# Kernel tuning notes

Hardware: AMD Instinct MI355X
Metric: run time of the kernel (lower is better)

Reference implementation:

```python
import jax, jax.numpy as jnp
import numpy as np

PUSH_MARGIN = 0.25


def setup_inputs() -> dict:
    key = jax.random.key(0)
    k1, k2 = jax.random.split(key)
    B, H, W, D, K = 8, 512, 512, 32, 64
    embeddings = jax.random.normal(k1, (B, H, W, D), dtype=jnp.float32)
    labels = jax.random.randint(k2, (B, H, W), 0, K, dtype=jnp.int32)
    return {"embeddings": embeddings, "labels": labels, "n_instances": K}


def _metric_loss(embeddings, labels, n_instances):
    # embeddings: (B, H, W, D) float; labels: (B, H, W) int; n_instances: static int K
    B = embeddings.shape[0]
    D = embeddings.shape[-1]
    K = n_instances
    emb = embeddings.reshape(B, -1, D)          # (B, N, D)
    lab = labels.reshape(B, -1).astype(jnp.int32)  # (B, N)

    # One-pass segment reduce over all batches: offset labels per batch element.
    seg = (lab + jnp.arange(B, dtype=jnp.int32)[:, None] * K).reshape(-1)  # (B*N,)
    sums = jax.ops.segment_sum(emb.reshape(-1, D), seg, num_segments=B * K)
    counts = jax.ops.segment_sum(jnp.ones(seg.shape, dtype=emb.dtype), seg,
                                 num_segments=B * K)
    sums = sums.reshape(B, K, D)
    counts = counts.reshape(B, K)
    present = counts > 0.5                       # non-empty instances (B, K)
    centroids = sums / jnp.maximum(counts, 1.0)[..., None]  # (B, K, D); zeros if empty

    # Pairwise Manhattan distances between centroids: (B, K, K)
    dist = jnp.sum(jnp.abs(centroids[:, :, None, :] - centroids[:, None, :, :]), axis=-1)
    hinge = jax.nn.relu(PUSH_MARGIN - dist)      # push: relu(margin - d)
    sq = hinge * hinge                           # squared error metric

    # strictly upper triangular + only pairs of non-empty instances
    triu = jnp.triu(jnp.ones((K, K), dtype=bool), k=1)
    pair_mask = triu[None] & present[:, :, None] & present[:, None, :]
    per_image_sum = jnp.sum(jnp.where(pair_mask, sq, 0.0), axis=(1, 2))  # (B,)

    n = jnp.sum(present.astype(emb.dtype), axis=1)              # (B,) non-empty count
    n_comparisons = n * (n - 1.0) / 2.0
    push_loss = per_image_sum / n_comparisons
    return jnp.mean(push_loss)


def reference(embeddings, labels, n_instances):
    return _metric_loss(embeddings, labels, n_instances)
```

## Files before the change

kernel.cpp:

```cpp
#include <hip/hip_runtime.h>

#define B_    8
#define N_    (512 * 512)
#define D_    32
#define K_    64
#define TPB   256
#define NWAVE (TPB / 64)
#define KROW  36
#define TABW  (K_ * KROW)
#define REC   (K_ * D_ + K_)
#define RECQ  (REC / 4)

#define PROC(L0,L1,L2,L3,L4,L5,L6,L7, V, PBASE)                               \
  {                                                                           \
    int lb = egl < 4 ? (egl < 2 ? (egl == 0 ? L0 : L1)                        \
                                : (egl == 2 ? L2 : L3))                       \
                     : (egl < 6 ? (egl == 4 ? L4 : L5)                        \
                                : (egl == 6 ? L6 : L7));                      \
    const int m0 = (lb == L0), m1 = (lb == L1), m2 = (lb == L2),              \
              m3 = (lb == L3), m4 = (lb == L4), m5 = (lb == L5),              \
              m6 = (lb == L6), m7 = (lb == L7);                               \
    const int order = (g0 & m0) + (g1 & m1) + (g2 & m2) + (g3 & m3) +         \
                      (g4 & m4) + (g5 & m5) + (g6 & m6);                      \
    const int nsame = m0 + m1 + m2 + m3 + m4 + m5 + m6 + m7;                  \
    const float4 vc = V;                                                      \
    const int pb = (PBASE);                                                   \
    if (pb < N_) {                                        \
      const int* lp = lab + bbase + pb + wb;      \
      L0 = lp[0]; L1 = lp[1]; L2 = lp[2]; L3 = lp[3];                         \
      L4 = lp[4]; L5 = lp[5]; L6 = lp[6]; L7 = lp[7];                         \
      V = embv[(bbase + pb + eg) * 8 + d4];                                   \
    }                                                                         \
    const int a = lb * KROW + d4 * 4;                                         \
    if (order == 0) {                                                         \
      float4 cur = *reinterpret_cast<const float4*>(tab + a);                 \
      cur.x += vc.x; cur.y += vc.y; cur.z += vc.z; cur.w += vc.w;             \
      *reinterpret_cast<float4*>(tab + a) = cur;                              \
      if (d4 == 0) cnt[lb] += (float)nsame;                                   \
    } else {                  \
      atomicAdd(&tab[a + 0], vc.x);                                           \
      atomicAdd(&tab[a + 1], vc.y);                                           \
      atomicAdd(&tab[a + 2], vc.z);                                           \
      atomicAdd(&tab[a + 3], vc.w);                                           \
    }                                                                         \
  }

__global__ __launch_bounds__(TPB) void seg_partial_kernel(
    const float* __restrict__ emb, const int* __restrict__ lab,
    float* __restrict__ partials, int blk_per_b)
{
    __shared__ __align__(16) float s_tab[NWAVE * TABW];
    __shared__ float s_cnt[NWAVE * K_];

    for (int i = threadIdx.x; i < NWAVE * TABW; i += TPB) s_tab[i] = 0.f;
    for (int i = threadIdx.x; i < NWAVE * K_;  i += TPB) s_cnt[i] = 0.f;
    __syncthreads();

    const int tid  = threadIdx.x;
    const int wave = tid >> 6;
    const int lane = tid & 63;
    const int egl  = lane >> 3;
    const int d4   = lane & 7;
    const int eg   = wave * 8 + egl;

    const int g0 = (0 < egl), g1 = (1 < egl), g2 = (2 < egl), g3 = (3 < egl),
              g4 = (4 < egl), g5 = (5 < egl), g6 = (6 < egl);

    float* __restrict__ tab = s_tab + wave * TABW;
    float* __restrict__ cnt = s_cnt + wave * K_;

    const int blk = blockIdx.x;
    const int b   = blk / blk_per_b;
    const int bib = blk - b * blk_per_b;
    const long long bbase = (long long)b * N_;
    const float4* __restrict__ embv = reinterpret_cast<const float4*>(emb);
    const int STEP = blk_per_b * 32;
    const int wb = __builtin_amdgcn_readfirstlane(wave * 8);

    int ib = bib * 32;

    int a0, a1, a2, a3, a4, a5, a6, a7;
    float4 va;
    {
        const int* lp = lab + bbase + ib + wb;
        a0 = lp[0]; a1 = lp[1]; a2 = lp[2]; a3 = lp[3];
        a4 = lp[4]; a5 = lp[5]; a6 = lp[6]; a7 = lp[7];
        va = embv[(bbase + ib + eg) * 8 + d4];
    }
    int b0 = 0, b1 = 0, b2 = 0, b3 = 0, b4 = 0, b5 = 0, b6 = 0, b7 = 0;
    float4 vb = make_float4(0.f, 0.f, 0.f, 0.f);
    if (ib + STEP < N_) {
        const int* lp = lab + bbase + ib + STEP + wb;
        b0 = lp[0]; b1 = lp[1]; b2 = lp[2]; b3 = lp[3];
        b4 = lp[4]; b5 = lp[5]; b6 = lp[6]; b7 = lp[7];
        vb = embv[(bbase + ib + STEP + eg) * 8 + d4];
    }

    for (;;) {
        PROC(a0, a1, a2, a3, a4, a5, a6, a7, va, ib + 2 * STEP);
        ib += STEP;
        if (ib >= N_) break;
        PROC(b0, b1, b2, b3, b4, b5, b6, b7, vb, ib + 2 * STEP);
        ib += STEP;
        if (ib >= N_) break;
    }
    __syncthreads();

    float* out = partials + (size_t)blk * REC;
    for (int i = tid; i < K_ * D_; i += TPB) {
        int k = i >> 5, d = i & 31;
        float s = 0.f;
#pragma unroll
        for (int w = 0; w < NWAVE; ++w) s += s_tab[w * TABW + k * KROW + d];
        out[i] = s;
    }
    if (tid < K_) {
        float c = 0.f;
#pragma unroll
        for (int w = 0; w < NWAVE; ++w) c += s_cnt[w * K_ + tid];
        out[K_ * D_ + tid] = c;
    }
}

__global__ __launch_bounds__(TPB) void seg_reduce_a(
    const float* __restrict__ partials, float* __restrict__ part2,
    int rpc, int nch)
{
    const int blk = blockIdx.x;
    const int b   = blk / nch;
    const int ch  = blk - b * nch;
    const int tid = threadIdx.x;

    const float4* __restrict__ p4 = reinterpret_cast<const float4*>(partials)
        + (size_t)((b * nch + ch) * rpc) * RECQ;
    float4* __restrict__ o4 = reinterpret_cast<float4*>(part2)
        + (size_t)blk * RECQ;

    float4 acc0 = make_float4(0.f, 0.f, 0.f, 0.f);
    float4 acc1 = acc0, acc2 = acc0;
#pragma unroll 4
    for (int r = 0; r < rpc; ++r) {
        const float4* rp = p4 + (size_t)r * RECQ;
        float4 v0 = rp[tid];
        float4 v1 = rp[tid + 256];
        acc0.x += v0.x; acc0.y += v0.y; acc0.z += v0.z; acc0.w += v0.w;
        acc1.x += v1.x; acc1.y += v1.y; acc1.z += v1.z; acc1.w += v1.w;
        if (tid < 16) {
            float4 v2 = rp[tid + 512];
            acc2.x += v2.x; acc2.y += v2.y; acc2.z += v2.z; acc2.w += v2.w;
        }
    }
    o4[tid]       = acc0;
    o4[tid + 256] = acc1;
    if (tid < 16) o4[tid + 512] = acc2;
}

__global__ __launch_bounds__(TPB) void loss8_kernel(
    const float* __restrict__ part2, float* __restrict__ batch_loss,
    int nch)
{
    __shared__ __align__(16) float4 s_cent4[8 * K_];
    __shared__ float s_cntsh[K_];
    __shared__ float s_pres[K_];
    __shared__ float s_wred[NWAVE];

    const int b   = blockIdx.x;
    const int tid = threadIdx.x;
    const float4* __restrict__ p4 = reinterpret_cast<const float4*>(part2)
        + (size_t)(b * nch) * RECQ;

    float4 acc0 = make_float4(0.f, 0.f, 0.f, 0.f);
    float4 acc1 = acc0, acc2 = acc0;
#pragma unroll 8
    for (int c = 0; c < nch; ++c) {
        const float4* rp = p4 + (size_t)c * RECQ;
        float4 v0 = rp[tid];
        float4 v1 = rp[tid + 256];
        acc0.x += v0.x; acc0.y += v0.y; acc0.z += v0.z; acc0.w += v0.w;
        acc1.x += v1.x; acc1.y += v1.y; acc1.z += v1.z; acc1.w += v1.w;
        if (tid < 16) {
            float4 v2 = rp[tid + 512];
            acc2.x += v2.x; acc2.y += v2.y; acc2.z += v2.z; acc2.w += v2.w;
        }
    }

    s_cent4[(tid & 7) * K_ + (tid >> 3)] = acc0;
    {
        const int q1 = tid + 256;
        s_cent4[(q1 & 7) * K_ + (q1 >> 3)] = acc1;
    }
    if (tid < 16) reinterpret_cast<float4*>(s_cntsh)[tid] = acc2;
    __syncthreads();

    if (tid < K_) s_pres[tid] = (s_cntsh[tid] > 0.5f) ? 1.f : 0.f;
    for (int i = tid; i < 8 * K_; i += TPB) {
        float inv = 1.0f / fmaxf(s_cntsh[i & 63], 1.0f);
        float4 c = s_cent4[i];
        c.x *= inv; c.y *= inv; c.z *= inv; c.w *= inv;
        s_cent4[i] = c;
    }
    __syncthreads();

    const int wave = tid >> 6, lane = tid & 63;

    float4 cb[8];
#pragma unroll
    for (int j = 0; j < 8; ++j) cb[j] = s_cent4[j * K_ + lane];
    const float pres2 = s_pres[lane];

    float acc = 0.f;
#pragma unroll 4
    for (int t = 0; t < 16; ++t) {
        const int k1 = wave * 16 + t;
        float dist = 0.f;
#pragma unroll
        for (int j = 0; j < 8; ++j) {
            float4 a = s_cent4[j * K_ + k1];
            dist += fabsf(a.x - cb[j].x) + fabsf(a.y - cb[j].y)
                  + fabsf(a.z - cb[j].z) + fabsf(a.w - cb[j].w);
        }
        float h = fmaxf(0.25f - dist, 0.f);
        float valid = (k1 < lane) ? s_pres[k1] * pres2 : 0.f;
        acc += valid * h * h;
    }
#pragma unroll
    for (int m = 32; m > 0; m >>= 1) acc += __shfl_xor(acc, m);
    if (lane == 0) s_wred[wave] = acc;
    __syncthreads();
    if (tid == 0) {
        float s = s_wred[0] + s_wred[1] + s_wred[2] + s_wred[3];
        float n = 0.f;
        for (int k = 0; k < K_; ++k) n += s_pres[k];
        float ncomp = n * (n - 1.f) * 0.5f;
        batch_loss[b] = (ncomp > 0.f) ? (s / ncomp) : 0.f;
    }
}

__global__ void final_kernel(const float* __restrict__ batch_loss,
                             float* __restrict__ out)
{
    if (threadIdx.x == 0) {
        float t = 0.f;
#pragma unroll
        for (int b = 0; b < B_; ++b) t += batch_loss[b];
        out[0] = t * (1.0f / (float)B_);
    }
}

extern "C" void kernel_launch(void* const* d_in, const int* in_sizes, int n_in,
                              void* d_out, int out_size, void* d_ws, size_t ws_size,
                              hipStream_t stream)
{
    const float* emb = (const float*)d_in[0];
    const int*   lab = (const int*)d_in[1];
    float*       out = (float*)d_out;
    float*       ws  = (float*)d_ws;

    int blk_per_b = 128;
    while (blk_per_b > 8) {
        size_t need = ((size_t)(blk_per_b * B_) * REC
                       + (size_t)(B_ * 8) * REC
                       + B_) * sizeof(float);
        if (need <= ws_size) break;
        blk_per_b >>= 1;
    }
    const int nblk = blk_per_b * B_;
    const int nch  = (blk_per_b >= 8) ? 8 : blk_per_b;
    const int rpc  = blk_per_b / nch;

    float* partials   = ws;
    float* part2      = ws + (size_t)nblk * REC;
    float* batch_loss = part2 + (size_t)(B_ * nch) * REC;

    seg_partial_kernel<<<nblk, TPB, 0, stream>>>(emb, lab, partials, blk_per_b);

    seg_reduce_a<<<B_ * nch, TPB, 0, stream>>>(partials, part2, rpc, nch);

    loss8_kernel<<<B_, TPB, 0, stream>>>(part2, batch_loss, nch);

    final_kernel<<<1, 64, 0, stream>>>(batch_loss, out);
}
```

Measured before the change: 74.72 us.

## Share shared-memory histogram tables between wave pairs and double blocks per batch

Each pair of waves now covers 16 pixels with 4 lanes per pixel per wave (the two waves split the 32 dims), so a block keeps two private centroid tables instead of four. This halves LDS usage, and together with launch_bounds(256,8) it is meant to raise occupancy. Counting moves to a per-pixel atomicAdd from a single designated lane, replacing the per-run count accumulation. Blocks per batch double to 256, which adds more partial records for the reduce stage to read. In exchange, the 16-way duplicate detection costs more ALU work and more label registers per thread.

```diff
diff --git a/kernel.cpp b/kernel.cpp
--- a/kernel.cpp
+++ b/kernel.cpp
@@ -6,37 +6,45 @@
 #define K_    64
 #define TPB   256
 #define NWAVE (TPB / 64)
+#define NPAIR (TPB / 128)
 #define KROW  36
 #define TABW  (K_ * KROW)
 #define REC   (K_ * D_ + K_)
 #define RECQ  (REC / 4)
 
-#define PROC(L0,L1,L2,L3,L4,L5,L6,L7, V, PBASE)                               \
+#define PROC16(L0,L1,L2,L3,L4,L5,L6,L7,L8,L9,L10,L11,L12,L13,L14,L15, V, PBASE) \
   {                                                                           \
-    int lb = egl < 4 ? (egl < 2 ? (egl == 0 ? L0 : L1)                        \
-                                : (egl == 2 ? L2 : L3))                       \
-                     : (egl < 6 ? (egl == 4 ? L4 : L5)                        \
-                                : (egl == 6 ? L6 : L7));                      \
-    const int m0 = (lb == L0), m1 = (lb == L1), m2 = (lb == L2),              \
-              m3 = (lb == L3), m4 = (lb == L4), m5 = (lb == L5),              \
-              m6 = (lb == L6), m7 = (lb == L7);                               \
+    int lb = el < 8                                                           \
+      ? (el < 4 ? (el < 2 ? (el == 0 ? L0 : L1) : (el == 2 ? L2 : L3))        \
+                : (el < 6 ? (el == 4 ? L4 : L5) : (el == 6 ? L6 : L7)))       \
+      : (el < 12 ? (el < 10 ? (el == 8 ? L8 : L9) : (el == 10 ? L10 : L11))   \
+                 : (el < 14 ? (el == 12 ? L12 : L13)                          \
+                            : (el == 14 ? L14 : L15)));                       \
+    const int m0 = (lb == L0),  m1 = (lb == L1),  m2 = (lb == L2),            \
+              m3 = (lb == L3),  m4 = (lb == L4),  m5 = (lb == L5),            \
+              m6 = (lb == L6),  m7 = (lb == L7),  m8 = (lb == L8),            \
+              m9 = (lb == L9),  m10 = (lb == L10), m11 = (lb == L11),         \
+              m12 = (lb == L12), m13 = (lb == L13), m14 = (lb == L14);        \
     const int order = (g0 & m0) + (g1 & m1) + (g2 & m2) + (g3 & m3) +         \
-                      (g4 & m4) + (g5 & m5) + (g6 & m6);                      \
-    const int nsame = m0 + m1 + m2 + m3 + m4 + m5 + m6 + m7;                  \
+                      (g4 & m4) + (g5 & m5) + (g6 & m6) + (g7 & m7) +         \
+                      (g8 & m8) + (g9 & m9) + (g10 & m10) + (g11 & m11) +     \
+                      (g12 & m12) + (g13 & m13) + (g14 & m14);                \
     const float4 vc = V;                                                      \
     const int pb = (PBASE);                                                   \
     if (pb < N_) {                                        \
       const int* lp = lab + bbase + pb + wb;      \
-      L0 = lp[0]; L1 = lp[1]; L2 = lp[2]; L3 = lp[3];                         \
-      L4 = lp[4]; L5 = lp[5]; L6 = lp[6]; L7 = lp[7];                         \
+      L0 = lp[0];  L1 = lp[1];  L2 = lp[2];  L3 = lp[3];                      \
+      L4 = lp[4];  L5 = lp[5];  L6 = lp[6];  L7 = lp[7];                      \
+      L8 = lp[8];  L9 = lp[9];  L10 = lp[10]; L11 = lp[11];                   \
+      L12 = lp[12]; L13 = lp[13]; L14 = lp[14]; L15 = lp[15];                 \
       V = embv[(bbase + pb + eg) * 8 + d4];                                   \
     }                                                                         \
     const int a = lb * KROW + d4 * 4;                                         \
+    if (czen) atomicAdd(&cnt[lb], 1.0f);                                      \
     if (order == 0) {                                                         \
       float4 cur = *reinterpret_cast<const float4*>(tab + a);                 \
       cur.x += vc.x; cur.y += vc.y; cur.z += vc.z; cur.w += vc.w;             \
       *reinterpret_cast<float4*>(tab + a) = cur;                              \
-      if (d4 == 0) cnt[lb] += (float)nsame;                                   \
     } else {                  \
       atomicAdd(&tab[a + 0], vc.x);                                           \
       atomicAdd(&tab[a + 1], vc.y);                                           \
@@ -45,29 +53,46 @@
     }                                                                         \
   }
 
-__global__ __launch_bounds__(TPB) void seg_partial_kernel(
+#define LOADSET16(L0,L1,L2,L3,L4,L5,L6,L7,L8,L9,L10,L11,L12,L13,L14,L15, V, BASE) \
+  if ((BASE) < N_) {                                                          \
+    const int* lp = lab + bbase + (BASE) + wb;                                \
+    L0 = lp[0];  L1 = lp[1];  L2 = lp[2];  L3 = lp[3];                        \
+    L4 = lp[4];  L5 = lp[5];  L6 = lp[6];  L7 = lp[7];                        \
+    L8 = lp[8];  L9 = lp[9];  L10 = lp[10]; L11 = lp[11];                     \
+    L12 = lp[12]; L13 = lp[13]; L14 = lp[14]; L15 = lp[15];                   \
+    V = embv[(bbase + (BASE) + eg) * 8 + d4];                                 \
+  }
+
+__global__ __launch_bounds__(TPB, 8) void seg_partial_kernel(
     const float* __restrict__ emb, const int* __restrict__ lab,
     float* __restrict__ partials, int blk_per_b)
 {
-    __shared__ __align__(16) float s_tab[NWAVE * TABW];
-    __shared__ float s_cnt[NWAVE * K_];
-
-    for (int i = threadIdx.x; i < NWAVE * TABW; i += TPB) s_tab[i] = 0.f;
-    for (int i = threadIdx.x; i < NWAVE * K_;  i += TPB) s_cnt[i] = 0.f;
+    __shared__ __align__(16) float s_tab[NPAIR * TABW];
+    __shared__ float s_cnt[NPAIR * K_];
+
+    for (int i = threadIdx.x; i < NPAIR * TABW; i += TPB) s_tab[i] = 0.f;
+    for (int i = threadIdx.x; i < NPAIR * K_;  i += TPB) s_cnt[i] = 0.f;
     __syncthreads();
 
     const int tid  = threadIdx.x;
     const int wave = tid >> 6;
+    const int pair = wave >> 1;
+    const int hi   = wave & 1;
     const int lane = tid & 63;
-    const int egl  = lane >> 3;
-    const int d4   = lane & 7;
-    const int eg   = wave * 8 + egl;
-
-    const int g0 = (0 < egl), g1 = (1 < egl), g2 = (2 < egl), g3 = (3 < egl),
-              g4 = (4 < egl), g5 = (5 < egl), g6 = (6 < egl);
-
-    float* __restrict__ tab = s_tab + wave * TABW;
-    float* __restrict__ cnt = s_cnt + wave * K_;
+    const int el   = lane >> 2;
+    const int q    = lane & 3;
+    const int d4   = q + 4 * hi;
+    const int eg   = pair * 16 + el;
+    const int czen = (hi == 0) && (q == 0);
+
+    const int g0 = (0 < el),  g1 = (1 < el),  g2 = (2 < el),  g3 = (3 < el),
+              g4 = (4 < el),  g5 = (5 < el),  g6 = (6 < el),  g7 = (7 < el),
+              g8 = (8 < el),  g9 = (9 < el),  g10 = (10 < el),
+              g11 = (11 < el), g12 = (12 < el), g13 = (13 < el),
+              g14 = (14 < el);
+
+    float* __restrict__ tab = s_tab + pair * TABW;
+    float* __restrict__ cnt = s_cnt + pair * K_;
 
     const int blk = blockIdx.x;
     const int b   = blk / blk_per_b;
@@ -75,32 +100,26 @@
     const long long bbase = (long long)b * N_;
     const float4* __restrict__ embv = reinterpret_cast<const float4*>(emb);
     const int STEP = blk_per_b * 32;
-    const int wb = __builtin_amdgcn_readfirstlane(wave * 8);
+    const int wb = __builtin_amdgcn_readfirstlane(pair * 16);
 
     int ib = bib * 32;
 
-    int a0, a1, a2, a3, a4, a5, a6, a7;
-    float4 va;
-    {
-        const int* lp = lab + bbase + ib + wb;
-        a0 = lp[0]; a1 = lp[1]; a2 = lp[2]; a3 = lp[3];
-        a4 = lp[4]; a5 = lp[5]; a6 = lp[6]; a7 = lp[7];
-        va = embv[(bbase + ib + eg) * 8 + d4];
-    }
-    int b0 = 0, b1 = 0, b2 = 0, b3 = 0, b4 = 0, b5 = 0, b6 = 0, b7 = 0;
-    float4 vb = make_float4(0.f, 0.f, 0.f, 0.f);
-    if (ib + STEP < N_) {
-        const int* lp = lab + bbase + ib + STEP + wb;
-        b0 = lp[0]; b1 = lp[1]; b2 = lp[2]; b3 = lp[3];
-        b4 = lp[4]; b5 = lp[5]; b6 = lp[6]; b7 = lp[7];
-        vb = embv[(bbase + ib + STEP + eg) * 8 + d4];
-    }
+    int a0 = 0, a1 = 0, a2 = 0, a3 = 0, a4 = 0, a5 = 0, a6 = 0, a7 = 0,
+        a8 = 0, a9 = 0, a10 = 0, a11 = 0, a12 = 0, a13 = 0, a14 = 0, a15 = 0;
+    int b0 = 0, b1 = 0, b2 = 0, b3 = 0, b4 = 0, b5 = 0, b6 = 0, b7 = 0,
+        b8 = 0, b9 = 0, b10 = 0, b11 = 0, b12 = 0, b13 = 0, b14 = 0, b15 = 0;
+    float4 va = make_float4(0.f, 0.f, 0.f, 0.f), vb = va;
+    LOADSET16(a0,a1,a2,a3,a4,a5,a6,a7,a8,a9,a10,a11,a12,a13,a14,a15, va, ib);
+    LOADSET16(b0,b1,b2,b3,b4,b5,b6,b7,b8,b9,b10,b11,b12,b13,b14,b15, vb,
+              ib + STEP);
 
     for (;;) {
-        PROC(a0, a1, a2, a3, a4, a5, a6, a7, va, ib + 2 * STEP);
+        PROC16(a0,a1,a2,a3,a4,a5,a6,a7,a8,a9,a10,a11,a12,a13,a14,a15, va,
+               ib + 2 * STEP);
         ib += STEP;
         if (ib >= N_) break;
-        PROC(b0, b1, b2, b3, b4, b5, b6, b7, vb, ib + 2 * STEP);
+        PROC16(b0,b1,b2,b3,b4,b5,b6,b7,b8,b9,b10,b11,b12,b13,b14,b15, vb,
+               ib + 2 * STEP);
         ib += STEP;
         if (ib >= N_) break;
     }
@@ -111,13 +130,13 @@
         int k = i >> 5, d = i & 31;
         float s = 0.f;
 #pragma unroll
-        for (int w = 0; w < NWAVE; ++w) s += s_tab[w * TABW + k * KROW + d];
+        for (int w = 0; w < NPAIR; ++w) s += s_tab[w * TABW + k * KROW + d];
         out[i] = s;
     }
     if (tid < K_) {
         float c = 0.f;
 #pragma unroll
-        for (int w = 0; w < NWAVE; ++w) c += s_cnt[w * K_ + tid];
+        for (int w = 0; w < NPAIR; ++w) c += s_cnt[w * K_ + tid];
         out[K_ * D_ + tid] = c;
     }
 }
@@ -256,7 +275,7 @@
     float*       out = (float*)d_out;
     float*       ws  = (float*)d_ws;
 
-    int blk_per_b = 128;
+    int blk_per_b = 256;
     while (blk_per_b > 8) {
         size_t need = ((size_t)(blk_per_b * B_) * REC
                        + (size_t)(B_ * 8) * REC
```

Result: slower. 107.5 us (+43.9%).

## Fuse reduce and loss kernels into one kernel using last-block atomic counters

Applied to the files above, without the earlier changes.

Merges the partial segment-sum, the two-level reduction, the per-image loss and the final mean into one kernel. Global atomic counters with threadfences pick the last-arriving block of each group to do the next reduction stage. This removes three extra kernel launches and the gaps between them, but adds a memset launch plus serialized tail work inside the last blocks.

```diff
diff --git a/kernel.cpp b/kernel.cpp
--- a/kernel.cpp
+++ b/kernel.cpp
@@ -10,6 +10,7 @@
 #define TABW  (K_ * KROW)
 #define REC   (K_ * D_ + K_)
 #define RECQ  (REC / 4)
+#define NGRP  (B_ * 8)
 
 #define PROC(L0,L1,L2,L3,L4,L5,L6,L7, V, PBASE)                               \
   {                                                                           \
@@ -45,12 +46,15 @@
     }                                                                         \
   }
 
-__global__ __launch_bounds__(TPB) void seg_partial_kernel(
+__global__ __launch_bounds__(TPB) void mono_kernel(
     const float* __restrict__ emb, const int* __restrict__ lab,
-    float* __restrict__ partials, int blk_per_b)
+    float* __restrict__ partials, float* __restrict__ part2,
+    float* __restrict__ batch_loss, int* __restrict__ counters,
+    float* __restrict__ out, int blk_per_b)
 {
     __shared__ __align__(16) float s_tab[NWAVE * TABW];
     __shared__ float s_cnt[NWAVE * K_];
+    __shared__ int   s_role;
 
     for (int i = threadIdx.x; i < NWAVE * TABW; i += TPB) s_tab[i] = 0.f;
     for (int i = threadIdx.x; i < NWAVE * K_;  i += TPB) s_cnt[i] = 0.f;
@@ -106,143 +110,149 @@
     }
     __syncthreads();
 
-    float* out = partials + (size_t)blk * REC;
+    float* outp = partials + (size_t)blk * REC;
     for (int i = tid; i < K_ * D_; i += TPB) {
         int k = i >> 5, d = i & 31;
         float s = 0.f;
 #pragma unroll
         for (int w = 0; w < NWAVE; ++w) s += s_tab[w * TABW + k * KROW + d];
-        out[i] = s;
+        outp[i] = s;
     }
     if (tid < K_) {
         float c = 0.f;
 #pragma unroll
         for (int w = 0; w < NWAVE; ++w) c += s_cnt[w * K_ + tid];
-        out[K_ * D_ + tid] = c;
-    }
-}
-
-__global__ __launch_bounds__(TPB) void seg_reduce_a(
-    const float* __restrict__ partials, float* __restrict__ part2,
-    int rpc, int nch)
-{
-    const int blk = blockIdx.x;
-    const int b   = blk / nch;
-    const int ch  = blk - b * nch;
-    const int tid = threadIdx.x;
-
-    const float4* __restrict__ p4 = reinterpret_cast<const float4*>(partials)
-        + (size_t)((b * nch + ch) * rpc) * RECQ;
-    float4* __restrict__ o4 = reinterpret_cast<float4*>(part2)
-        + (size_t)blk * RECQ;
-
-    float4 acc0 = make_float4(0.f, 0.f, 0.f, 0.f);
-    float4 acc1 = acc0, acc2 = acc0;
+        outp[K_ * D_ + tid] = c;
+    }
+
+    const int gsize = blk_per_b >> 3;
+    const int g     = blk / gsize;
+
+    __syncthreads();
+    if (tid == 0) {
+        __threadfence();
+        s_role = (atomicAdd(&counters[g], 1) == gsize - 1);
+    }
+    __syncthreads();
+    if (!s_role) return;
+    __threadfence();
+
+    {
+        const float4* __restrict__ p4 = reinterpret_cast<const float4*>(partials)
+            + (size_t)(g * gsize) * RECQ;
+        float4* __restrict__ o4 = reinterpret_cast<float4*>(part2)
+            + (size_t)g * RECQ;
+        float4 acc0 = make_float4(0.f, 0.f, 0.f, 0.f);
+        float4 acc1 = acc0, acc2 = acc0;
 #pragma unroll 4
-    for (int r = 0; r < rpc; ++r) {
-        const float4* rp = p4 + (size_t)r * RECQ;
-        float4 v0 = rp[tid];
-        float4 v1 = rp[tid + 256];
-        acc0.x += v0.x; acc0.y += v0.y; acc0.z += v0.z; acc0.w += v0.w;
-        acc1.x += v1.x; acc1.y += v1.y; acc1.z += v1.z; acc1.w += v1.w;
-        if (tid < 16) {
-            float4 v2 = rp[tid + 512];
-            acc2.x += v2.x; acc2.y += v2.y; acc2.z += v2.z; acc2.w += v2.w;
-        }
-    }
-    o4[tid]       = acc0;
-    o4[tid + 256] = acc1;
-    if (tid < 16) o4[tid + 512] = acc2;
-}
-
-__global__ __launch_bounds__(TPB) void loss8_kernel(
-    const float* __restrict__ part2, float* __restrict__ batch_loss,
-    int nch)
-{
-    __shared__ __align__(16) float4 s_cent4[8 * K_];
-    __shared__ float s_cntsh[K_];
-    __shared__ float s_pres[K_];
-    __shared__ float s_wred[NWAVE];
-
-    const int b   = blockIdx.x;
-    const int tid = threadIdx.x;
-    const float4* __restrict__ p4 = reinterpret_cast<const float4*>(part2)
-        + (size_t)(b * nch) * RECQ;
-
-    float4 acc0 = make_float4(0.f, 0.f, 0.f, 0.f);
-    float4 acc1 = acc0, acc2 = acc0;
+        for (int r = 0; r < gsize; ++r) {
+            const float4* rp = p4 + (size_t)r * RECQ;
+            float4 v0 = rp[tid];
+            float4 v1 = rp[tid + 256];
+            acc0.x += v0.x; acc0.y += v0.y; acc0.z += v0.z; acc0.w += v0.w;
+            acc1.x += v1.x; acc1.y += v1.y; acc1.z += v1.z; acc1.w += v1.w;
+            if (tid < 16) {
+                float4 v2 = rp[tid + 512];
+                acc2.x += v2.x; acc2.y += v2.y; acc2.z += v2.z; acc2.w += v2.w;
+            }
+        }
+        o4[tid]       = acc0;
+        o4[tid + 256] = acc1;
+        if (tid < 16) o4[tid + 512] = acc2;
+    }
+    __syncthreads();
+    if (tid == 0) {
+        __threadfence();
+        s_role = (atomicAdd(&counters[NGRP + b], 1) == 7);
+    }
+    __syncthreads();
+    if (!s_role) return;
+    __threadfence();
+
+    {
+        float4* s_cent4 = reinterpret_cast<float4*>(s_tab);
+        float*  s_cntsh = s_tab + 2048;
+        float*  s_pres  = s_tab + 2112;
+        float*  s_wred  = s_tab + 2176;
+
+        const float4* __restrict__ p4 = reinterpret_cast<const float4*>(part2)
+            + (size_t)(b * 8) * RECQ;
+
+        float4 acc0 = make_float4(0.f, 0.f, 0.f, 0.f);
+        float4 acc1 = acc0, acc2 = acc0;
 #pragma unroll 8
-    for (int c = 0; c < nch; ++c) {
-        const float4* rp = p4 + (size_t)c * RECQ;
-        float4 v0 = rp[tid];
-        float4 v1 = rp[tid + 256];
-        acc0.x += v0.x; acc0.y += v0.y; acc0.z += v0.z; acc0.w += v0.w;
-        acc1.x += v1.x; acc1.y += v1.y; acc1.z += v1.z; acc1.w += v1.w;
-        if (tid < 16) {
-            float4 v2 = rp[tid + 512];
-            acc2.x += v2.x; acc2.y += v2.y; acc2.z += v2.z; acc2.w += v2.w;
-        }
-    }
-
-    s_cent4[(tid & 7) * K_ + (tid >> 3)] = acc0;
-    {
-        const int q1 = tid + 256;
-        s_cent4[(q1 & 7) * K_ + (q1 >> 3)] = acc1;
-    }
-    if (tid < 16) reinterpret_cast<float4*>(s_cntsh)[tid] = acc2;
-    __syncthreads();
-
-    if (tid < K_) s_pres[tid] = (s_cntsh[tid] > 0.5f) ? 1.f : 0.f;
-    for (int i = tid; i < 8 * K_; i += TPB) {
-        float inv = 1.0f / fmaxf(s_cntsh[i & 63], 1.0f);
-        float4 c = s_cent4[i];
-        c.x *= inv; c.y *= inv; c.z *= inv; c.w *= inv;
-        s_cent4[i] = c;
-    }
-    __syncthreads();
-
-    const int wave = tid >> 6, lane = tid & 63;
-
-    float4 cb[8];
-#pragma unroll
-    for (int j = 0; j < 8; ++j) cb[j] = s_cent4[j * K_ + lane];
-    const float pres2 = s_pres[lane];
-
-    float acc = 0.f;
+        for (int c = 0; c < 8; ++c) {
+            const float4* rp = p4 + (size_t)c * RECQ;
+            float4 v0 = rp[tid];
+            float4 v1 = rp[tid + 256];
+            acc0.x += v0.x; acc0.y += v0.y; acc0.z += v0.z; acc0.w += v0.w;
+            acc1.x += v1.x; acc1.y += v1.y; acc1.z += v1.z; acc1.w += v1.w;
+            if (tid < 16) {
+                float4 v2 = rp[tid + 512];
+                acc2.x += v2.x; acc2.y += v2.y; acc2.z += v2.z; acc2.w += v2.w;
+            }
+        }
+        __syncthreads();
+
+        s_cent4[(tid & 7) * K_ + (tid >> 3)] = acc0;
+        {
+            const int q1 = tid + 256;
+            s_cent4[(q1 & 7) * K_ + (q1 >> 3)] = acc1;
+        }
+        if (tid < 16) reinterpret_cast<float4*>(s_cntsh)[tid] = acc2;
+        __syncthreads();
+
+        if (tid < K_) s_pres[tid] = (s_cntsh[tid] > 0.5f) ? 1.f : 0.f;
+        for (int i = tid; i < 8 * K_; i += TPB) {
+            float inv = 1.0f / fmaxf(s_cntsh[i & 63], 1.0f);
+            float4 c = s_cent4[i];
+            c.x *= inv; c.y *= inv; c.z *= inv; c.w *= inv;
+            s_cent4[i] = c;
+        }
+        __syncthreads();
+
+        float4 cb[8];
+#pragma unroll
+        for (int j = 0; j < 8; ++j) cb[j] = s_cent4[j * K_ + lane];
+        const float pres2 = s_pres[lane];
+
+        float acc = 0.f;
 #pragma unroll 4
-    for (int t = 0; t < 16; ++t) {
-        const int k1 = wave * 16 + t;
-        float dist = 0.f;
-#pragma unroll
-        for (int j = 0; j < 8; ++j) {
-            float4 a = s_cent4[j * K_ + k1];
-            dist += fabsf(a.x - cb[j].x) + fabsf(a.y - cb[j].y)
-                  + fabsf(a.z - cb[j].z) + fabsf(a.w - cb[j].w);
-        }
-        float h = fmaxf(0.25f - dist, 0.f);
-        float valid = (k1 < lane) ? s_pres[k1] * pres2 : 0.f;
-        acc += valid * h * h;
-    }
-#pragma unroll
-    for (int m = 32; m > 0; m >>= 1) acc += __shfl_xor(acc, m);
-    if (lane == 0) s_wred[wave] = acc;
-    __syncthreads();
+        for (int t = 0; t < 16; ++t) {
+            const int k1 = wave * 16 + t;
+            float dist = 0.f;
+#pragma unroll
+            for (int j = 0; j < 8; ++j) {
+                float4 a = s_cent4[j * K_ + k1];
+                dist += fabsf(a.x - cb[j].x) + fabsf(a.y - cb[j].y)
+                      + fabsf(a.z - cb[j].z) + fabsf(a.w - cb[j].w);
+            }
+            float h = fmaxf(0.25f - dist, 0.f);
+            float valid = (k1 < lane) ? s_pres[k1] * pres2 : 0.f;
+            acc += valid * h * h;
+        }
+#pragma unroll
+        for (int m = 32; m > 0; m >>= 1) acc += __shfl_xor(acc, m);
+        if (lane == 0) s_wred[wave] = acc;
+        __syncthreads();
+        if (tid == 0) {
+            float s = s_wred[0] + s_wred[1] + s_wred[2] + s_wred[3];
+            float n = 0.f;
+            for (int k = 0; k < K_; ++k) n += s_pres[k];
+            float ncomp = n * (n - 1.f) * 0.5f;
+            batch_loss[b] = (ncomp > 0.f) ? (s / ncomp) : 0.f;
+            __threadfence();
+            s_role = (atomicAdd(&counters[NGRP + B_], 1) == B_ - 1);
+        }
+    }
+    __syncthreads();
+    if (!s_role) return;
+
     if (tid == 0) {
-        float s = s_wred[0] + s_wred[1] + s_wred[2] + s_wred[3];
-        float n = 0.f;
-        for (int k = 0; k < K_; ++k) n += s_pres[k];
-        float ncomp = n * (n - 1.f) * 0.5f;
-        batch_loss[b] = (ncomp > 0.f) ? (s / ncomp) : 0.f;
-    }
-}
-
-__global__ void final_kernel(const float* __restrict__ batch_loss,
-                             float* __restrict__ out)
-{
-    if (threadIdx.x == 0) {
+        __threadfence();
         float t = 0.f;
 #pragma unroll
-        for (int b = 0; b < B_; ++b) t += batch_loss[b];
+        for (int bb = 0; bb < B_; ++bb) t += batch_loss[bb];
         out[0] = t * (1.0f / (float)B_);
     }
 }
@@ -259,24 +269,21 @@
     int blk_per_b = 128;
     while (blk_per_b > 8) {
         size_t need = ((size_t)(blk_per_b * B_) * REC
-                       + (size_t)(B_ * 8) * REC
-                       + B_) * sizeof(float);
+                       + (size_t)NGRP * REC
+                       + B_) * sizeof(float)
+                      + (NGRP + B_ + 1) * sizeof(int);
         if (need <= ws_size) break;
         blk_per_b >>= 1;
     }
     const int nblk = blk_per_b * B_;
-    const int nch  = (blk_per_b >= 8) ? 8 : blk_per_b;
-    const int rpc  = blk_per_b / nch;
 
     float* partials   = ws;
     float* part2      = ws + (size_t)nblk * REC;
-    float* batch_loss = part2 + (size_t)(B_ * nch) * REC;
-
-    seg_partial_kernel<<<nblk, TPB, 0, stream>>>(emb, lab, partials, blk_per_b);
-
-    seg_reduce_a<<<B_ * nch, TPB, 0, stream>>>(partials, part2, rpc, nch);
-
-    loss8_kernel<<<B_, TPB, 0, stream>>>(part2, batch_loss, nch);
-
-    final_kernel<<<1, 64, 0, stream>>>(batch_loss, out);
+    float* batch_loss = part2 + (size_t)NGRP * REC;
+    int*   counters   = (int*)(batch_loss + B_);
+
+    hipMemsetAsync(counters, 0, (NGRP + B_ + 1) * sizeof(int), stream);
+
+    mono_kernel<<<nblk, TPB, 0, stream>>>(emb, lab, partials, part2,
+                                          batch_loss, counters, out, blk_per_b);
 }
```

After: 228.5 us. 3.06x slower.
